# Kernel optimization log

Measured on AMD Instinct MI355X. Metric: run time of the kernel, lower is better.

## Reference

```python
import jax, jax.numpy as jnp
import numpy as np

EPS_LAM = 1e-6
GN_GROUPS = 4
GN_EPS = 1e-5


def _conv(x, k):
    # x: (N, Cin, H, W), k: (Cout, Cin, 3, 3), SAME padding, stride 1
    return jax.lax.conv_general_dilated(x, k, (1, 1), 'SAME',
                                        dimension_numbers=('NCHW', 'OIHW', 'NCHW'))


def _clifford_conv(x, wa, wb, ba, bb):
    # Cl(0,1) (complex-style) Clifford conv: channels split into two blade components.
    C = x.shape[1]
    h = C // 2
    a, b = x[:, :h], x[:, h:]
    oa = _conv(a, wa) - _conv(b, wb) + ba[None, :, None, None]
    ob = _conv(a, wb) + _conv(b, wa) + bb[None, :, None, None]
    return jnp.concatenate([oa, ob], axis=1)


def _helmholtz(x):
    # Project the vector field (vx = first half of channels, vy = second half)
    # onto its divergence-free component in Fourier space.
    N, C, H, W = x.shape
    h = C // 2
    vx, vy = x[:, :h], x[:, h:]
    kx = jnp.fft.rfftfreq(W)[None, :]   # (1, FW)
    ky = jnp.fft.fftfreq(H)[:, None]    # (H, 1)
    k2 = kx * kx + ky * ky              # (H, FW)
    vxh = jnp.fft.rfft2(vx, norm='ortho')
    vyh = jnp.fft.rfft2(vy, norm='ortho')
    num = kx * vxh + ky * vyh
    p = jnp.where(k2 == 0, 0.0, num / jnp.where(k2 == 0, 1.0, k2))
    vxp = jnp.fft.irfft2(vxh - kx * p, s=(H, W), norm='ortho')
    vyp = jnp.fft.irfft2(vyh - ky * p, s=(H, W), norm='ortho')
    return jnp.concatenate([vxp, vyp], axis=1)


def _group_norm(x, w, b):
    N, C, H, W = x.shape
    xg = x.reshape(N, GN_GROUPS, -1)
    mu = xg.mean(-1, keepdims=True)
    var = xg.var(-1, keepdims=True)
    xn = ((xg - mu) * jax.lax.rsqrt(var + GN_EPS)).reshape(N, C, H, W)
    return xn * w[None, :, None, None] + b[None, :, None, None]


def setup_inputs() -> dict:
    key = jax.random.key(0)
    ks = jax.random.split(key, 6)
    B, T, C, H, W = 2, 16, 128, 64, 64
    hC = C // 2
    sc = 0.05
    return {
        'x_seq': jax.random.normal(ks[0], (B, T, C, H, W), jnp.float32),
        'dt_seq': jax.random.uniform(ks[1], (B, T), jnp.float32, 0.05, 1.0),
        'gen_w': jax.random.normal(ks[2], (C, 2 * C), jnp.float32) * (1.0 / np.sqrt(C)),
        'gen_b': jnp.zeros((2 * C,), jnp.float32),
        'cw_a': jax.random.normal(ks[3], (hC, hC, 3, 3), jnp.float32) * sc,
        'cw_b': jax.random.normal(ks[4], (hC, hC, 3, 3), jnp.float32) * sc,
        'cb_a': jnp.zeros((hC,), jnp.float32),
        'cb_b': jnp.zeros((hC,), jnp.float32),
        'gn_w': jnp.ones((C,), jnp.float32),
        'gn_b': jnp.zeros((C,), jnp.float32),
    }


def reference(x_seq, dt_seq, gen_w, gen_b, cw_a, cw_b, cb_a, cb_b, gn_w, gn_b):
    B, T, C, H, W = x_seq.shape
    dt = dt_seq[:, :, None, None, None]                   # (B,T,1,1,1)
    x_fft = jnp.fft.rfft2(x_seq, norm='ortho')            # (B,T,C,H,FW) complex64
    stats = x_seq.mean(axis=(-1, -2))                     # (B,T,C)
    params = stats @ gen_w + gen_b                        # (B,T,2C)
    nu, omega = jnp.split(params, 2, axis=-1)
    lam = (-jnp.abs(nu) + 1j * omega)[:, :, :, None, None]  # (B,T,C,1,1)
    A_scan = jnp.exp(lam * dt)
    small = jnp.abs(lam) < EPS_LAM
    safe = jnp.where(small, jnp.complex64(EPS_LAM), lam)
    X_term = jnp.where(small, dt.astype(jnp.complex64), (jnp.exp(safe * dt) - 1.0) / safe)
    X = (x_fft * X_term).astype(jnp.complex64)            # (B,T,C,H,FW)
    A = jnp.broadcast_to(A_scan.astype(jnp.complex64), X.shape)

    def comb(l, r):
        al, xl = l
        ar, xr = r
        return (al * ar, ar * xl + xr)

    _, h_fft = jax.lax.associative_scan(comb, (A, X), axis=1)  # h_t = A_t h_{t-1} + X_t
    h = jnp.fft.irfft2(h_fft, s=(H, W), norm='ortho')
    hf = h.reshape(B * T, C, H, W)
    u = hf + _clifford_conv(hf, cw_a, cw_b, cb_a, cb_b)
    u = _helmholtz(u)
    out = _group_norm(u, gn_w, gn_b)
    return out.reshape(B, T, C, H, W)
```

## Files before the change

kernel.cpp:

```cpp
#include <hip/hip_runtime.h>
#include <math.h>

#define PI_F 3.14159265358979323846f
#define ST 66

typedef __attribute__((ext_vector_type(8))) short short8;
typedef __attribute__((ext_vector_type(4))) float f32x4;
typedef __attribute__((ext_vector_type(4))) unsigned short u16x4;
typedef __attribute__((ext_vector_type(8))) unsigned short u16x8;

static __device__ __forceinline__ int sw(int row, int intra) {
    return row * ST + (intra ^ (row & 7));
}

static __device__ __forceinline__ unsigned short f2bf(float x) {
    unsigned u = __float_as_uint(x);
    unsigned r = (u + 0x7FFF + ((u >> 16) & 1)) >> 16;
    return (unsigned short)r;
}
static __device__ __forceinline__ float bf2f(unsigned short u) {
    return __uint_as_float(((unsigned)u) << 16);
}
static __device__ __forceinline__ float2 unpk(unsigned v) {
    return make_float2(bf2f((unsigned short)(v & 0xffff)), bf2f((unsigned short)(v >> 16)));
}

static __device__ __forceinline__ float2 cadd(float2 a, float2 b) { return make_float2(a.x + b.x, a.y + b.y); }
static __device__ __forceinline__ float2 csub(float2 a, float2 b) { return make_float2(a.x - b.x, a.y - b.y); }
static __device__ __forceinline__ float2 cmul(float2 a, float2 b) { return make_float2(a.x * b.x - a.y * b.y, a.x * b.y + a.y * b.x); }
static __device__ __forceinline__ float2 cmulc(float2 a, float2 b) { return make_float2(a.x * b.x + a.y * b.y, a.y * b.x - a.x * b.y); }

template <int S>
static __device__ __forceinline__ void dft8(float2* z) {
    const float RT = 0.70710678118654752440f;
    float2 ee0 = cadd(z[0], z[4]), ee1 = csub(z[0], z[4]);
    float2 eo0 = cadd(z[2], z[6]), eo1 = csub(z[2], z[6]);
    float2 oe0 = cadd(z[1], z[5]), oe1 = csub(z[1], z[5]);
    float2 oo0 = cadd(z[3], z[7]), oo1 = csub(z[3], z[7]);
    float2 ieo1 = make_float2(-S * eo1.y, S * eo1.x);
    float2 ioo1 = make_float2(-S * oo1.y, S * oo1.x);
    float2 E0 = cadd(ee0, eo0), E2 = csub(ee0, eo0);
    float2 E1 = cadd(ee1, ieo1), E3 = csub(ee1, ieo1);
    float2 O0 = cadd(oe0, oo0), O2 = csub(oe0, oo0);
    float2 O1 = cadd(oe1, ioo1), O3 = csub(oe1, ioo1);
    float2 w1O1 = make_float2(RT * (O1.x - S * O1.y), RT * (S * O1.x + O1.y));
    float2 w3O3 = make_float2(RT * (-O3.x - S * O3.y), RT * (S * O3.x - O3.y));
    float2 iO2  = make_float2(-S * O2.y, S * O2.x);
    z[0] = cadd(E0, O0);   z[4] = csub(E0, O0);
    z[1] = cadd(E1, w1O1); z[5] = csub(E1, w1O1);
    z[2] = cadd(E2, iO2);  z[6] = csub(E2, iO2);
    z[3] = cadd(E3, w3O3); z[7] = csub(E3, w3O3);
}

template <int S>
static __device__ __forceinline__ void fftRowsA(float2* G, const float2* twl, int tid) {
#pragma unroll
    for (int sl = 0; sl < 2; ++sl) {
        int s = tid + sl * 256;
        int row = s >> 3, b = s & 7;
        float2 z[8];
#pragma unroll
        for (int a = 0; a < 8; ++a) z[a] = G[sw(row, 8 * a + b)];
        dft8<S>(z);
#pragma unroll
        for (int c = 0; c < 8; ++c) {
            float2 t = twl[(b * c) & 63];
            G[sw(row, 8 * c + b)] = (S < 0) ? cmul(z[c], t) : cmulc(z[c], t);
        }
    }
}
template <int S>
static __device__ __forceinline__ void fftRowsB(float2* G, int tid) {
    int r0 = tid >> 3, c = tid & 7, r1 = r0 + 32;
    float2 z0[8], z1[8];
#pragma unroll
    for (int b = 0; b < 8; ++b) z0[b] = G[sw(r0, 8 * c + b)];
#pragma unroll
    for (int b = 0; b < 8; ++b) z1[b] = G[sw(r1, 8 * c + b)];
    dft8<S>(z0); dft8<S>(z1);
    __syncthreads();
#pragma unroll
    for (int d = 0; d < 8; ++d) G[sw(r0, c + 8 * d)] = z0[d];
#pragma unroll
    for (int d = 0; d < 8; ++d) G[sw(r1, c + 8 * d)] = z1[d];
}
template <int S>
static __device__ __forceinline__ void fftColsA(float2* G, const float2* twl, int tid) {
#pragma unroll
    for (int sl = 0; sl < 2; ++sl) {
        int s = tid + sl * 256;
        int col = s & 63, b = s >> 6;
        float2 z[8];
#pragma unroll
        for (int a = 0; a < 8; ++a) z[a] = G[sw(8 * a + b, col)];
        dft8<S>(z);
#pragma unroll
        for (int c = 0; c < 8; ++c) {
            float2 t = twl[(b * c) & 63];
            G[sw(8 * c + b, col)] = (S < 0) ? cmul(z[c], t) : cmulc(z[c], t);
        }
    }
}
template <int S>
static __device__ __forceinline__ void fftColsB(float2* G, int tid) {
    int col = tid & 63, c0 = tid >> 6, c1 = c0 + 4;
    float2 z0[8], z1[8];
#pragma unroll
    for (int b = 0; b < 8; ++b) z0[b] = G[sw(8 * c0 + b, col)];
#pragma unroll
    for (int b = 0; b < 8; ++b) z1[b] = G[sw(8 * c1 + b, col)];
    dft8<S>(z0); dft8<S>(z1);
    __syncthreads();
#pragma unroll
    for (int d = 0; d < 8; ++d) G[sw(c0 + 8 * d, col)] = z0[d];
#pragma unroll
    for (int d = 0; d < 8; ++d) G[sw(c1 + 8 * d, col)] = z1[d];
}

__global__ __launch_bounds__(256) void k_params(const float* __restrict__ stats,
                                                const float* __restrict__ gw,
                                                const float* __restrict__ gb,
                                                const float* __restrict__ dts,
                                                float2* __restrict__ A,
                                                float2* __restrict__ Xt) {
    int idx = blockIdx.x * 256 + threadIdx.x;
    int c = idx & 127;
    int bt = idx >> 7;
    const float* st = stats + bt * 128;
    float nu = gb[c], om = gb[c + 128];
    for (int k = 0; k < 128; ++k) {
        float s = st[k];
        nu += s * gw[k * 256 + c];
        om += s * gw[k * 256 + c + 128];
    }
    float dt = dts[bt];
    float lre = -fabsf(nu);
    float lim = om;
    float mag = sqrtf(lre * lre + lim * lim);
    float er = expf(lre * dt);
    float sn, cs;
    sincosf(lim * dt, &sn, &cs);
    float2 Av = make_float2(er * cs, er * sn);
    float2 X;
    if (mag < 1e-6f) {
        X = make_float2(dt, 0.f);
    } else {
        float ar = Av.x - 1.f, ai = Av.y;
        float inv = 1.f / (mag * mag);
        X = make_float2((ar * lre + ai * lim) * inv, (ai * lre - ar * lim) * inv);
    }
    A[idx] = Av;
    Xt[idx] = X;
}

__global__ __launch_bounds__(256) void k_rfft2s(const float* __restrict__ xin,
                                                unsigned* __restrict__ Sb,
                                                float* __restrict__ stats) {
    int p = blockIdx.x, tid = threadIdx.x;
    __shared__ float2 G[64 * ST], twl[64];
    __shared__ float red[8];
    if (tid < 64) {
        float sn, cs;
        sincosf(-(2.0f * PI_F / 64.0f) * (float)tid, &sn, &cs);
        twl[tid] = make_float2(cs, sn);
    }
    const float* x0 = xin + (size_t)(2 * p) * 4096;
    const float* x1 = x0 + 4096;
    float s0 = 0.f, s1 = 0.f;
    for (int i4 = tid; i4 < 1024; i4 += 256) {
        float4 a = ((const float4*)x0)[i4];
        float4 b = ((const float4*)x1)[i4];
        s0 += a.x + a.y + a.z + a.w;
        s1 += b.x + b.y + b.z + b.w;
        int r = i4 >> 4, w = (i4 & 15) << 2;
        G[sw(r, w + 0)] = make_float2(a.x, b.x);
        G[sw(r, w + 1)] = make_float2(a.y, b.y);
        G[sw(r, w + 2)] = make_float2(a.z, b.z);
        G[sw(r, w + 3)] = make_float2(a.w, b.w);
    }
    for (int off = 32; off > 0; off >>= 1) {
        s0 += __shfl_xor(s0, off, 64);
        s1 += __shfl_xor(s1, off, 64);
    }
    if ((tid & 63) == 0) { red[(tid >> 6) * 2] = s0; red[(tid >> 6) * 2 + 1] = s1; }
    __syncthreads();
    if (tid < 2) {
        float t = red[tid] + red[tid + 2] + red[tid + 4] + red[tid + 6];
        stats[2 * p + tid] = t * (1.0f / 4096.0f);
    }
    fftRowsA<-1>(G, twl, tid); __syncthreads();
    fftRowsB<-1>(G, tid);      __syncthreads();
    fftColsA<-1>(G, twl, tid); __syncthreads();
    fftColsB<-1>(G, tid);      __syncthreads();

    unsigned* o0 = Sb + (size_t)(2 * p) * 2112;
    unsigned* o1 = o0 + 2112;
    for (int i = tid; i < 2112; i += 256) {
        int my = i / 33, mx = i - my * 33;
        float2 Zk = G[sw(my, mx)];
        float2 Zm = G[sw((64 - my) & 63, (64 - mx) & 63)];
        float a0 = (Zk.x + Zm.x) * (0.5f / 64.0f);
        float a1 = (Zk.y - Zm.y) * (0.5f / 64.0f);
        float b0 = (Zk.y + Zm.y) * (0.5f / 64.0f);
        float b1 = (Zm.x - Zk.x) * (0.5f / 64.0f);
        o0[i] = (unsigned)f2bf(a0) | ((unsigned)f2bf(a1) << 16);
        o1[i] = (unsigned)f2bf(b0) | ((unsigned)f2bf(b1) << 16);
    }
}

typedef __attribute__((ext_vector_type(2))) unsigned uint2v;
__global__ __launch_bounds__(256) void k_scan(unsigned* __restrict__ Sb,
                                              const float2* __restrict__ A,
                                              const float2* __restrict__ Xt) {
    int tid = blockIdx.x * 256 + threadIdx.x;
    int s = tid % 1056;
    int c = (tid / 1056) & 127;
    int b = tid / (1056 * 128);
    float2 h0 = make_float2(0.f, 0.f), h1 = make_float2(0.f, 0.f);
    for (int t = 0; t < 16; ++t) {
        int bt = b * 16 + t;
        float2 a = A[bt * 128 + c];
        float2 xt = Xt[bt * 128 + c];
        size_t off = ((size_t)(bt * 128 + c)) * 2112 + 2 * s;
        uint2v v = *(uint2v*)(Sb + off);
        float2 x0 = cmul(unpk(v[0]), xt);
        float2 x1 = cmul(unpk(v[1]), xt);
        h0 = make_float2(a.x * h0.x - a.y * h0.y + x0.x, a.x * h0.y + a.y * h0.x + x0.y);
        h1 = make_float2(a.x * h1.x - a.y * h1.y + x1.x, a.x * h1.y + a.y * h1.x + x1.y);
        uint2v o;
        o[0] = (unsigned)f2bf(h0.x) | ((unsigned)f2bf(h0.y) << 16);
        o[1] = (unsigned)f2bf(h1.x) | ((unsigned)f2bf(h1.y) << 16);
        *(uint2v*)(Sb + off) = o;
    }
}

__global__ __launch_bounds__(256) void k_irfft2b(const unsigned* __restrict__ Sb,
                                                 unsigned short* __restrict__ hb) {
    int p = blockIdx.x, tid = threadIdx.x;
    __shared__ float2 G[64 * ST], twl[64];
    if (tid < 64) {
        float sn, cs;
        sincosf(-(2.0f * PI_F / 64.0f) * (float)tid, &sn, &cs);
        twl[tid] = make_float2(cs, sn);
    }
    const unsigned* i0 = Sb + (size_t)(2 * p) * 2112;
    const unsigned* i1 = i0 + 2112;
    for (int i = tid; i < 1984; i += 256) {
        int mx = 1 + i % 31, my = i / 31;
        int idx = my * 33 + mx;
        float2 a = unpk(i0[idx]);
        float2 b = unpk(i1[idx]);
        G[sw(my, mx)] = make_float2(a.x - b.y, a.y + b.x);
        G[sw((64 - my) & 63, 64 - mx)] = make_float2(a.x + b.y, b.x - a.y);
    }
    if (tid < 64) {
        int mx = (tid >= 32) ? 32 : 0;
        int r = tid & 31;
        if (r == 0) {
#pragma unroll
            for (int q = 0; q < 2; ++q) {
                int my = q * 32;
                float2 a = unpk(i0[my * 33 + mx]);
                float2 b = unpk(i1[my * 33 + mx]);
                G[sw(my, mx)] = make_float2(a.x, b.x);
            }
        } else {
            int my = r, my2 = 64 - r;
            float2 A0 = unpk(i0[my * 33 + mx]),  B0 = unpk(i0[my2 * 33 + mx]);
            float2 A1 = unpk(i1[my * 33 + mx]),  B1 = unpk(i1[my2 * 33 + mx]);
            float2 V0 = make_float2((A0.x + B0.x) * 0.5f, (A0.y - B0.y) * 0.5f);
            float2 V1 = make_float2((A1.x + B1.x) * 0.5f, (A1.y - B1.y) * 0.5f);
            G[sw(my, mx)]  = make_float2(V0.x - V1.y, V0.y + V1.x);
            G[sw(my2, mx)] = make_float2(V0.x + V1.y, V1.x - V0.y);
        }
    }
    __syncthreads();
    fftColsA<1>(G, twl, tid); __syncthreads();
    fftColsB<1>(G, tid);      __syncthreads();
    fftRowsA<1>(G, twl, tid); __syncthreads();
    fftRowsB<1>(G, tid);      __syncthreads();

    unsigned short* h0 = hb + (size_t)(2 * p) * 4096;
    unsigned short* h1 = h0 + 4096;
    for (int i4 = tid; i4 < 1024; i4 += 256) {
        int r = i4 >> 4, w = (i4 & 15) << 2;
        u16x4 oa, ob;
#pragma unroll
        for (int e = 0; e < 4; ++e) {
            float2 v = G[sw(r, w + e)];
            oa[e] = f2bf(v.x * (1.0f / 64.0f));
            ob[e] = f2bf(v.y * (1.0f / 64.0f));
        }
        ((u16x4*)h0)[i4] = oa;
        ((u16x4*)h1)[i4] = ob;
    }
}

__global__ __launch_bounds__(256) void k_wprep(const float* __restrict__ cwa,
                                               const float* __restrict__ cwb,
                                               unsigned short* __restrict__ Wb) {
    int idx = blockIdx.x * 256 + threadIdx.x;
    int kl = idx & 31;
    int m = (idx >> 5) & 127;
    int tcb = idx >> 12;
    int cb = tcb & 3, t = tcb >> 2;
    int ci = cb * 32 + kl;
    int mm = m & 63, cc = ci & 63;
    float w;
    if (m < 64) w = (ci < 64) ? cwa[(mm * 64 + cc) * 9 + t] : -cwb[(mm * 64 + cc) * 9 + t];
    else        w = (ci < 64) ? cwb[(mm * 64 + cc) * 9 + t] :  cwa[(mm * 64 + cc) * 9 + t];
    if (m == ci && t == 4) w += 1.0f;
    Wb[idx] = f2bf(w);
}

__global__ __launch_bounds__(256, 2) void k_conv_mfma(const unsigned short* __restrict__ hb,
                                                      const unsigned short* __restrict__ Wb,
                                                      const float* __restrict__ cba,
                                                      const float* __restrict__ cbb,
                                                      unsigned short* __restrict__ uout) {
    __shared__ __align__(16) char smem[65536];
    int f = blockIdx.y;
    int r0 = blockIdx.x * 2;
    int tid = threadIdx.x;
    const unsigned short* base = hb + (size_t)f * 524288;

    int wid = tid >> 6, lane = tid & 63;
    int lhi = lane >> 4, llo = lane & 15;
    int row_off = wid & 1;
    int mbase = (wid >> 1) * 64;

    auto ldA = [&](int t, int cb, short8* a) {
        const unsigned short* wp = Wb + ((size_t)((t * 4 + cb) * 128 + mbase + llo)) * 32 + lhi * 8;
#pragma unroll
        for (int mf = 0; mf < 4; ++mf) a[mf] = *(const short8*)(wp + mf * 16 * 32);
    };
    auto ldB = [&](int t, int cb, short8* b) {
        int dy = t / 3 - 1, dx = t % 3 - 1;
        int prow = row_off + 1 + dy;
        int slot = cb * 4 + lhi;
#pragma unroll
        for (int nf = 0; nf < 4; ++nf) {
            int c = nf * 16 + llo;
            int cdx = c + dx;
            bool valid = ((unsigned)cdx < 64u);
            int cr = valid ? cdx : c;
            int byteoff = ((prow * 64 + cr) << 8) + ((slot ^ (cr & 15)) << 4);
            short8 bb = *(const short8*)(smem + byteoff);
            b[nf] = valid ? bb : (short8)0;
        }
    };

    short8 aC[4], bC[4], aN[4], bN[4];
    ldA(0, 0, aC);

    for (int j = tid; j < 4096; j += 256) {
        int row = j >> 10;
        int cig = (j >> 6) & 15;
        int col = j & 63;
        int gr = r0 - 1 + row;
        short8 v = (short8)0;
        if ((unsigned)gr < 64u) {
            const unsigned short* p = base + (size_t)(cig * 8) * 4096 + gr * 64 + col;
#pragma unroll
            for (int e = 0; e < 8; ++e) v[e] = (short)p[(size_t)e * 4096];
        }
        int byteoff = ((row * 64 + col) << 8) + ((cig ^ (col & 15)) << 4);
        *(short8*)(smem + byteoff) = v;
    }
    __syncthreads();

    f32x4 acc[4][4];
#pragma unroll
    for (int mf = 0; mf < 4; ++mf)
#pragma unroll
        for (int nf = 0; nf < 4; ++nf) acc[mf][nf] = (f32x4)0.f;

    ldB(0, 0, bC);
#pragma unroll
    for (int it = 0; it < 36; ++it) {
        if (it < 35) {
            int tn = (it + 1) >> 2, cbn = (it + 1) & 3;
            ldA(tn, cbn, aN);
            ldB(tn, cbn, bN);
        }
        __builtin_amdgcn_s_setprio(1);
#pragma unroll
        for (int mf = 0; mf < 4; ++mf)
#pragma unroll
            for (int nf = 0; nf < 4; ++nf)
                acc[mf][nf] = __builtin_amdgcn_mfma_f32_16x16x32_bf16(aC[mf], bC[nf], acc[mf][nf], 0, 0, 0);
        __builtin_amdgcn_s_setprio(0);
#pragma unroll
        for (int k = 0; k < 4; ++k) { aC[k] = aN[k]; bC[k] = bN[k]; }
    }

    int grow = r0 + row_off;
#pragma unroll
    for (int mf = 0; mf < 4; ++mf) {
#pragma unroll
        for (int r = 0; r < 4; ++r) {
            int co = mbase + mf * 16 + lhi * 4 + r;
            float bias = (co < 64) ? cba[co] : cbb[co - 64];
            unsigned short* op = uout + ((size_t)f * 128 + co) * 4096 + (size_t)grow * 64;
#pragma unroll
            for (int nf = 0; nf < 4; ++nf)
                op[nf * 16 + llo] = f2bf(acc[mf][nf][r] + bias);
        }
    }
}

__global__ __launch_bounds__(256) void k_helm(const unsigned short* __restrict__ uin,
                                              unsigned short* __restrict__ uo,
                                              float* __restrict__ partials) {
    int bid = blockIdx.x;
    int f = bid >> 6, c = bid & 63;
    int tid = threadIdx.x;
    __shared__ float2 G[64 * ST], twl[64];
    __shared__ float red[16];
    if (tid < 64) {
        float sn, cs;
        sincosf(-(2.0f * PI_F / 64.0f) * (float)tid, &sn, &cs);
        twl[tid] = make_float2(cs, sn);
    }
    const unsigned short* u0 = uin + ((size_t)f * 128 + c) * 4096;
    const unsigned short* u1 = u0 + (size_t)64 * 4096;
    for (int i4 = tid; i4 < 1024; i4 += 256) {
        u16x4 a = ((const u16x4*)u0)[i4];
        u16x4 b = ((const u16x4*)u1)[i4];
        int r = i4 >> 4, w = (i4 & 15) << 2;
#pragma unroll
        for (int e = 0; e < 4; ++e)
            G[sw(r, w + e)] = make_float2(bf2f(a[e]), bf2f(b[e]));
    }
    __syncthreads();
    fftRowsA<-1>(G, twl, tid); __syncthreads();
    fftRowsB<-1>(G, tid);      __syncthreads();
    fftColsA<-1>(G, twl, tid); __syncthreads();
    fftColsB<-1>(G, tid);      __syncthreads();

    for (int i = tid; i < 1984; i += 256) {
        int mx = 1 + i % 31, my = i / 31;
        float2 Zk = G[sw(my, mx)];
        float2 Zm = G[sw((64 - my) & 63, 64 - mx)];
        float2 Vx = make_float2((Zk.x + Zm.x) * 0.5f, (Zk.y - Zm.y) * 0.5f);
        float2 Vy = make_float2((Zk.y + Zm.y) * 0.5f, (Zm.x - Zk.x) * 0.5f);
        float fx = (float)mx * (1.0f / 64.0f);
        float fy = (float)(my < 32 ? my : my - 64) * (1.0f / 64.0f);
        float inv = 1.0f / (fx * fx + fy * fy);
        float Pr = (fx * Vx.x + fy * Vy.x) * inv;
        float Pi = (fx * Vx.y + fy * Vy.y) * inv;
        Vx.x -= fx * Pr; Vx.y -= fx * Pi;
        Vy.x -= fy * Pr; Vy.y -= fy * Pi;
        G[sw(my, mx)] = make_float2(Vx.x - Vy.y, Vx.y + Vy.x);
        G[sw((64 - my) & 63, 64 - mx)] = make_float2(Vx.x + Vy.y, Vy.x - Vx.y);
    }
    if (tid < 64) {
        int mx = (tid >= 32) ? 32 : 0;
        int r = tid & 31;
        float fx = (float)mx * (1.0f / 64.0f);
        if (r == 0) {
#pragma unroll
            for (int q = 0; q < 2; ++q) {
                int my = q * 32;
                float fy = (my == 0) ? 0.f : -0.5f;
                float k2 = fx * fx + fy * fy;
                float2 Z = G[sw(my, mx)];
                float vx = Z.x, vy = Z.y;
                if (k2 > 0.f) {
                    float P = (fx * vx + fy * vy) / k2;
                    vx -= fx * P; vy -= fy * P;
                }
                G[sw(my, mx)] = make_float2(vx, vy);
            }
        } else {
            int my = r, my2 = 64 - r;
            float fy = (float)my * (1.0f / 64.0f);
            float inv = 1.0f / (fx * fx + fy * fy);
            float2 Zk = G[sw(my, mx)];
            float2 Zm = G[sw(my2, mx)];
            float2 Vx = make_float2((Zk.x + Zm.x) * 0.5f, (Zk.y - Zm.y) * 0.5f);
            float2 Vy = make_float2((Zk.y + Zm.y) * 0.5f, (Zm.x - Zk.x) * 0.5f);
            float Pr = (fx * Vx.x + fy * Vy.x) * inv;
            float Pi = (fx * Vx.y + fy * Vy.y) * inv;
            float2 Xk = make_float2(Vx.x - fx * Pr, Vx.y - fx * Pi);
            float2 Yk = make_float2(Vy.x - fy * Pr, Vy.y - fy * Pi);
            float P2r = (fx * Vx.x - fy * Vy.x) * inv;
            float P2i = (-fx * Vx.y + fy * Vy.y) * inv;
            float2 Xk2 = make_float2(Vx.x - fx * P2r, -Vx.y - fx * P2i);
            float2 Yk2 = make_float2(Vy.x + fy * P2r, -Vy.y + fy * P2i);
            float2 Xh = make_float2((Xk.x + Xk2.x) * 0.5f, (Xk.y - Xk2.y) * 0.5f);
            float2 Yh = make_float2((Yk.x + Yk2.x) * 0.5f, (Yk.y - Yk2.y) * 0.5f);
            G[sw(my, mx)]  = make_float2(Xh.x - Yh.y, Xh.y + Yh.x);
            G[sw(my2, mx)] = make_float2(Xh.x + Yh.y, Yh.x - Xh.y);
        }
    }
    __syncthreads();
    fftColsA<1>(G, twl, tid); __syncthreads();
    fftColsB<1>(G, tid);      __syncthreads();
    fftRowsA<1>(G, twl, tid); __syncthreads();
    fftRowsB<1>(G, tid);      __syncthreads();

    unsigned short* o0 = uo + ((size_t)f * 128 + c) * 4096;
    unsigned short* o1 = o0 + (size_t)64 * 4096;
    float s0 = 0.f, q0 = 0.f, s1 = 0.f, q1 = 0.f;
    for (int i4 = tid; i4 < 1024; i4 += 256) {
        int r = i4 >> 4, w = (i4 & 15) << 2;
        u16x4 oa, ob;
#pragma unroll
        for (int e = 0; e < 4; ++e) {
            float2 v = G[sw(r, w + e)];
            float a = v.x * (1.0f / 4096.0f);
            float b = v.y * (1.0f / 4096.0f);
            s0 += a; q0 += a * a; s1 += b; q1 += b * b;
            oa[e] = f2bf(a); ob[e] = f2bf(b);
        }
        ((u16x4*)o0)[i4] = oa;
        ((u16x4*)o1)[i4] = ob;
    }
    for (int off = 32; off > 0; off >>= 1) {
        s0 += __shfl_xor(s0, off, 64); q0 += __shfl_xor(q0, off, 64);
        s1 += __shfl_xor(s1, off, 64); q1 += __shfl_xor(q1, off, 64);
    }
    if ((tid & 63) == 0) {
        int w6 = tid >> 6;
        red[w6 * 4 + 0] = s0; red[w6 * 4 + 1] = q0;
        red[w6 * 4 + 2] = s1; red[w6 * 4 + 3] = q1;
    }
    __syncthreads();
    if (tid == 0) {
        float S0 = 0.f, Q0 = 0.f, S1 = 0.f, Q1 = 0.f;
#pragma unroll
        for (int w6 = 0; w6 < 4; ++w6) {
            S0 += red[w6 * 4 + 0]; Q0 += red[w6 * 4 + 1];
            S1 += red[w6 * 4 + 2]; Q1 += red[w6 * 4 + 3];
        }
        float* pp = partials + ((size_t)f * 64 + c) * 4;
        pp[0] = S0; pp[1] = Q0; pp[2] = S1; pp[3] = Q1;
    }
}

__global__ __launch_bounds__(128) void k_gnfin(const float* __restrict__ partials,
                                               float2* __restrict__ gs) {
    int i = threadIdx.x;
    int f = i >> 2, g = i & 3;
    const float4* p4 = (const float4*)partials;
    float s = 0.f, q = 0.f;
    if (g < 2) {
        for (int cc = 0; cc < 32; ++cc) {
            float4 p = p4[f * 64 + g * 32 + cc];
            s += p.x; q += p.y;
        }
    } else {
        for (int cc = 0; cc < 32; ++cc) {
            float4 p = p4[f * 64 + (g - 2) * 32 + cc];
            s += p.z; q += p.w;
        }
    }
    float mu = s * (1.0f / 131072.0f);
    float var = q * (1.0f / 131072.0f) - mu * mu;
    gs[i] = make_float2(mu, rsqrtf(var + 1e-5f));
}

__global__ __launch_bounds__(256) void k_gnapply(const unsigned short* __restrict__ u,
                                                 const float2* __restrict__ gs,
                                                 const float* __restrict__ gnw,
                                                 const float* __restrict__ gnb,
                                                 float* __restrict__ out) {
    size_t i8 = (size_t)blockIdx.x * 256 + threadIdx.x;
    u16x8 v = ((const u16x8*)u)[i8];
    int cl = (int)(i8 >> 9);
    int c = cl & 127;
    int fg = cl >> 5;
    float2 ms = gs[fg];
    float sc = ms.y * gnw[c];
    float sh = gnb[c] - ms.x * sc;
    float4 r0, r1;
    r0.x = bf2f(v[0]) * sc + sh; r0.y = bf2f(v[1]) * sc + sh;
    r0.z = bf2f(v[2]) * sc + sh; r0.w = bf2f(v[3]) * sc + sh;
    r1.x = bf2f(v[4]) * sc + sh; r1.y = bf2f(v[5]) * sc + sh;
    r1.z = bf2f(v[6]) * sc + sh; r1.w = bf2f(v[7]) * sc + sh;
    ((float4*)out)[i8 * 2]     = r0;
    ((float4*)out)[i8 * 2 + 1] = r1;
}

extern "C" void kernel_launch(void* const* d_in, const int* in_sizes, int n_in,
                              void* d_out, int out_size, void* d_ws, size_t ws_size,
                              hipStream_t stream) {
    (void)in_sizes; (void)n_in; (void)out_size; (void)ws_size;
    const float* x   = (const float*)d_in[0];
    const float* dts = (const float*)d_in[1];
    const float* gw  = (const float*)d_in[2];
    const float* gb  = (const float*)d_in[3];
    const float* cwa = (const float*)d_in[4];
    const float* cwb = (const float*)d_in[5];
    const float* cba = (const float*)d_in[6];
    const float* cbb = (const float*)d_in[7];
    const float* gnw = (const float*)d_in[8];
    const float* gnb = (const float*)d_in[9];
    float* out = (float*)d_out;
    char* ws = (char*)d_ws;

    unsigned*       Sb  = (unsigned*)ws;
    unsigned short* Hb  = (unsigned short*)(ws + 34603008);
    unsigned short* Ub  = (unsigned short*)(ws + 68157440);
    unsigned short* H1b = (unsigned short*)(ws + 101711872);
    float*  stats    = (float*)(ws + 135266304);
    float2* A        = (float2*)(ws + 135282688);
    float2* Xt       = (float2*)(ws + 135315456);
    float2* gs       = (float2*)(ws + 135348224);
    float*  partials = (float*)(ws + 135349248);
    unsigned short* Wb = (unsigned short*)ws;

    k_rfft2s<<<2048, 256, 0, stream>>>(x, Sb, stats);
    k_params<<<16, 256, 0, stream>>>(stats, gw, gb, dts, A, Xt);
    k_scan<<<1056, 256, 0, stream>>>(Sb, A, Xt);
    k_irfft2b<<<2048, 256, 0, stream>>>(Sb, Hb);
    k_wprep<<<576, 256, 0, stream>>>(cwa, cwb, Wb);
    k_conv_mfma<<<dim3(32, 32), 256, 0, stream>>>(Hb, Wb, cba, cbb, Ub);
    k_helm<<<2048, 256, 0, stream>>>(Ub, H1b, partials);
    k_gnfin<<<1, 128, 0, stream>>>(partials, gs);
    k_gnapply<<<8192, 256, 0, stream>>>(H1b, gs, gnw, gnb, out);
}
```

Baseline: 213.0 us.

## Make 2D FFT passes wave-local to replace block barriers with wave syncs

Reassigns FFT work so each wavefront owns 16 complete rows (or columns) and does both radix-8 stages on them. The intermediate block-wide barriers inside each 1D pass become wave-level LDS waitcnt fences, and the load/store loops are remapped so each wave touches only its own rows. This removes several __syncthreads per FFT in the rfft, irfft and Helmholtz kernels, and adds per-wave twiddle copies plus a rotated column read order to reduce bank conflicts. The risk is that correctness now depends on the wave-size and LDS-ordering assumptions behind wave_sync.

```diff
diff --git a/kernel.cpp b/kernel.cpp
--- a/kernel.cpp
+++ b/kernel.cpp
@@ -8,9 +8,15 @@
 typedef __attribute__((ext_vector_type(4))) float f32x4;
 typedef __attribute__((ext_vector_type(4))) unsigned short u16x4;
 typedef __attribute__((ext_vector_type(8))) unsigned short u16x8;
+typedef __attribute__((ext_vector_type(2))) unsigned uint2v;
 
 static __device__ __forceinline__ int sw(int row, int intra) {
     return row * ST + (intra ^ (row & 7));
+}
+
+static __device__ __forceinline__ void wave_sync() {
+    asm volatile("s_waitcnt lgkmcnt(0)" ::: "memory");
+    __builtin_amdgcn_sched_barrier(0);
 }
 
 static __device__ __forceinline__ unsigned short f2bf(float x) {
@@ -53,11 +59,12 @@
 }
 
 template <int S>
-static __device__ __forceinline__ void fftRowsA(float2* G, const float2* twl, int tid) {
+static __device__ __forceinline__ void waveRows(float2* G, const float2* twl, int w, int lane) {
+    int lr = lane >> 3, b = lane & 7;
+    int r0 = 16 * w + lr;
 #pragma unroll
     for (int sl = 0; sl < 2; ++sl) {
-        int s = tid + sl * 256;
-        int row = s >> 3, b = s & 7;
+        int row = r0 + 8 * sl;
         float2 z[8];
 #pragma unroll
         for (int a = 0; a < 8; ++a) z[a] = G[sw(row, 8 * a + b)];
@@ -68,28 +75,29 @@
             G[sw(row, 8 * c + b)] = (S < 0) ? cmul(z[c], t) : cmulc(z[c], t);
         }
     }
+    wave_sync();
+    {
+        int c = b;
+        float2 z0[8], z1[8];
+#pragma unroll
+        for (int q = 0; q < 8; ++q) z0[q] = G[sw(r0, c * 8 + q)];
+#pragma unroll
+        for (int q = 0; q < 8; ++q) z1[q] = G[sw(r0 + 8, c * 8 + q)];
+        dft8<S>(z0); dft8<S>(z1);
+        wave_sync();
+#pragma unroll
+        for (int d = 0; d < 8; ++d) G[sw(r0, c + 8 * d)] = z0[d];
+#pragma unroll
+        for (int d = 0; d < 8; ++d) G[sw(r0 + 8, c + 8 * d)] = z1[d];
+    }
 }
 template <int S>
-static __device__ __forceinline__ void fftRowsB(float2* G, int tid) {
-    int r0 = tid >> 3, c = tid & 7, r1 = r0 + 32;
-    float2 z0[8], z1[8];
-#pragma unroll
-    for (int b = 0; b < 8; ++b) z0[b] = G[sw(r0, 8 * c + b)];
-#pragma unroll
-    for (int b = 0; b < 8; ++b) z1[b] = G[sw(r1, 8 * c + b)];
-    dft8<S>(z0); dft8<S>(z1);
-    __syncthreads();
-#pragma unroll
-    for (int d = 0; d < 8; ++d) G[sw(r0, c + 8 * d)] = z0[d];
-#pragma unroll
-    for (int d = 0; d < 8; ++d) G[sw(r1, c + 8 * d)] = z1[d];
-}
-template <int S>
-static __device__ __forceinline__ void fftColsA(float2* G, const float2* twl, int tid) {
+static __device__ __forceinline__ void waveCols(float2* G, const float2* twl, int w, int lane) {
+    int cl = lane >> 3, b = lane & 7;
+    int c0 = 16 * w + cl;
 #pragma unroll
     for (int sl = 0; sl < 2; ++sl) {
-        int s = tid + sl * 256;
-        int col = s & 63, b = s >> 6;
+        int col = c0 + 8 * sl;
         float2 z[8];
 #pragma unroll
         for (int a = 0; a < 8; ++a) z[a] = G[sw(8 * a + b, col)];
@@ -100,21 +108,27 @@
             G[sw(8 * c + b, col)] = (S < 0) ? cmul(z[c], t) : cmulc(z[c], t);
         }
     }
-}
-template <int S>
-static __device__ __forceinline__ void fftColsB(float2* G, int tid) {
-    int col = tid & 63, c0 = tid >> 6, c1 = c0 + 4;
-    float2 z0[8], z1[8];
-#pragma unroll
-    for (int b = 0; b < 8; ++b) z0[b] = G[sw(8 * c0 + b, col)];
-#pragma unroll
-    for (int b = 0; b < 8; ++b) z1[b] = G[sw(8 * c1 + b, col)];
-    dft8<S>(z0); dft8<S>(z1);
-    __syncthreads();
-#pragma unroll
-    for (int d = 0; d < 8; ++d) G[sw(c0 + 8 * d, col)] = z0[d];
-#pragma unroll
-    for (int d = 0; d < 8; ++d) G[sw(c1 + 8 * d, col)] = z1[d];
+    wave_sync();
+    {
+        int cidx = b;
+        float2 z0[8], z1[8];
+#pragma unroll
+        for (int q = 0; q < 8; ++q) {
+            int b2 = (q + cidx) & 7;
+            z0[b2] = G[sw(8 * cidx + b2, c0)];
+        }
+#pragma unroll
+        for (int q = 0; q < 8; ++q) {
+            int b2 = (q + cidx) & 7;
+            z1[b2] = G[sw(8 * cidx + b2, c0 + 8)];
+        }
+        dft8<S>(z0); dft8<S>(z1);
+        wave_sync();
+#pragma unroll
+        for (int d = 0; d < 8; ++d) G[sw(cidx + 8 * d, c0)] = z0[d];
+#pragma unroll
+        for (int d = 0; d < 8; ++d) G[sw(cidx + 8 * d, c0 + 8)] = z1[d];
+    }
 }
 
 __global__ __launch_bounds__(256) void k_params(const float* __restrict__ stats,
@@ -157,6 +171,7 @@
                                                 unsigned* __restrict__ Sb,
                                                 float* __restrict__ stats) {
     int p = blockIdx.x, tid = threadIdx.x;
+    int w = tid >> 6, lane = tid & 63;
     __shared__ float2 G[64 * ST], twl[64];
     __shared__ float red[8];
     if (tid < 64) {
@@ -172,26 +187,26 @@
         float4 b = ((const float4*)x1)[i4];
         s0 += a.x + a.y + a.z + a.w;
         s1 += b.x + b.y + b.z + b.w;
-        int r = i4 >> 4, w = (i4 & 15) << 2;
-        G[sw(r, w + 0)] = make_float2(a.x, b.x);
-        G[sw(r, w + 1)] = make_float2(a.y, b.y);
-        G[sw(r, w + 2)] = make_float2(a.z, b.z);
-        G[sw(r, w + 3)] = make_float2(a.w, b.w);
+        int r = i4 >> 4, wv = (i4 & 15) << 2;
+        G[sw(r, wv + 0)] = make_float2(a.x, b.x);
+        G[sw(r, wv + 1)] = make_float2(a.y, b.y);
+        G[sw(r, wv + 2)] = make_float2(a.z, b.z);
+        G[sw(r, wv + 3)] = make_float2(a.w, b.w);
     }
     for (int off = 32; off > 0; off >>= 1) {
         s0 += __shfl_xor(s0, off, 64);
         s1 += __shfl_xor(s1, off, 64);
     }
-    if ((tid & 63) == 0) { red[(tid >> 6) * 2] = s0; red[(tid >> 6) * 2 + 1] = s1; }
+    if (lane == 0) { red[w * 2] = s0; red[w * 2 + 1] = s1; }
     __syncthreads();
     if (tid < 2) {
         float t = red[tid] + red[tid + 2] + red[tid + 4] + red[tid + 6];
         stats[2 * p + tid] = t * (1.0f / 4096.0f);
     }
-    fftRowsA<-1>(G, twl, tid); __syncthreads();
-    fftRowsB<-1>(G, tid);      __syncthreads();
-    fftColsA<-1>(G, twl, tid); __syncthreads();
-    fftColsB<-1>(G, tid);      __syncthreads();
+    waveRows<-1>(G, twl, w, lane);
+    __syncthreads();
+    waveCols<-1>(G, twl, w, lane);
+    __syncthreads();
 
     unsigned* o0 = Sb + (size_t)(2 * p) * 2112;
     unsigned* o1 = o0 + 2112;
@@ -208,7 +223,6 @@
     }
 }
 
-typedef __attribute__((ext_vector_type(2))) unsigned uint2v;
 __global__ __launch_bounds__(256) void k_scan(unsigned* __restrict__ Sb,
                                               const float2* __restrict__ A,
                                               const float2* __restrict__ Xt) {
@@ -237,6 +251,7 @@
 __global__ __launch_bounds__(256) void k_irfft2b(const unsigned* __restrict__ Sb,
                                                  unsigned short* __restrict__ hb) {
     int p = blockIdx.x, tid = threadIdx.x;
+    int w = tid >> 6, lane = tid & 63;
     __shared__ float2 G[64 * ST], twl[64];
     if (tid < 64) {
         float sn, cs;
@@ -275,24 +290,24 @@
         }
     }
     __syncthreads();
-    fftColsA<1>(G, twl, tid); __syncthreads();
-    fftColsB<1>(G, tid);      __syncthreads();
-    fftRowsA<1>(G, twl, tid); __syncthreads();
-    fftRowsB<1>(G, tid);      __syncthreads();
+    waveCols<1>(G, twl, w, lane);
+    __syncthreads();
+    waveRows<1>(G, twl, w, lane);
+    wave_sync();
 
     unsigned short* h0 = hb + (size_t)(2 * p) * 4096;
     unsigned short* h1 = h0 + 4096;
-    for (int i4 = tid; i4 < 1024; i4 += 256) {
-        int r = i4 >> 4, w = (i4 & 15) << 2;
+    for (int j = lane; j < 256; j += 64) {
+        int row = 16 * w + (j >> 4), ch = j & 15;
         u16x4 oa, ob;
 #pragma unroll
         for (int e = 0; e < 4; ++e) {
-            float2 v = G[sw(r, w + e)];
+            float2 v = G[sw(row, ch * 4 + e)];
             oa[e] = f2bf(v.x * (1.0f / 64.0f));
             ob[e] = f2bf(v.y * (1.0f / 64.0f));
         }
-        ((u16x4*)h0)[i4] = oa;
-        ((u16x4*)h1)[i4] = ob;
+        ((u16x4*)h0)[row * 16 + ch] = oa;
+        ((u16x4*)h1)[row * 16 + ch] = ob;
     }
 }
 
@@ -415,28 +430,31 @@
     int bid = blockIdx.x;
     int f = bid >> 6, c = bid & 63;
     int tid = threadIdx.x;
-    __shared__ float2 G[64 * ST], twl[64];
+    int w = tid >> 6, lane = tid & 63;
+    __shared__ float2 G[64 * ST], twl4[256];
     __shared__ float red[16];
-    if (tid < 64) {
+    {
         float sn, cs;
-        sincosf(-(2.0f * PI_F / 64.0f) * (float)tid, &sn, &cs);
-        twl[tid] = make_float2(cs, sn);
-    }
+        sincosf(-(2.0f * PI_F / 64.0f) * (float)lane, &sn, &cs);
+        twl4[w * 64 + lane] = make_float2(cs, sn);
+    }
+    const float2* twl = twl4 + w * 64;
+
     const unsigned short* u0 = uin + ((size_t)f * 128 + c) * 4096;
     const unsigned short* u1 = u0 + (size_t)64 * 4096;
-    for (int i4 = tid; i4 < 1024; i4 += 256) {
-        u16x4 a = ((const u16x4*)u0)[i4];
-        u16x4 b = ((const u16x4*)u1)[i4];
-        int r = i4 >> 4, w = (i4 & 15) << 2;
+    for (int j = lane; j < 256; j += 64) {
+        int row = 16 * w + (j >> 4), ch = j & 15;
+        u16x4 a = ((const u16x4*)u0)[row * 16 + ch];
+        u16x4 b = ((const u16x4*)u1)[row * 16 + ch];
 #pragma unroll
         for (int e = 0; e < 4; ++e)
-            G[sw(r, w + e)] = make_float2(bf2f(a[e]), bf2f(b[e]));
-    }
-    __syncthreads();
-    fftRowsA<-1>(G, twl, tid); __syncthreads();
-    fftRowsB<-1>(G, tid);      __syncthreads();
-    fftColsA<-1>(G, twl, tid); __syncthreads();
-    fftColsB<-1>(G, tid);      __syncthreads();
+            G[sw(row, ch * 4 + e)] = make_float2(bf2f(a[e]), bf2f(b[e]));
+    }
+    wave_sync();
+    waveRows<-1>(G, twl, w, lane);
+    __syncthreads();
+    waveCols<-1>(G, twl, w, lane);
+    __syncthreads();
 
     for (int i = tid; i < 1984; i += 256) {
         int mx = 1 + i % 31, my = i / 31;
@@ -495,36 +513,35 @@
         }
     }
     __syncthreads();
-    fftColsA<1>(G, twl, tid); __syncthreads();
-    fftColsB<1>(G, tid);      __syncthreads();
-    fftRowsA<1>(G, twl, tid); __syncthreads();
-    fftRowsB<1>(G, tid);      __syncthreads();
+    waveCols<1>(G, twl, w, lane);
+    __syncthreads();
+    waveRows<1>(G, twl, w, lane);
+    wave_sync();
 
     unsigned short* o0 = uo + ((size_t)f * 128 + c) * 4096;
     unsigned short* o1 = o0 + (size_t)64 * 4096;
     float s0 = 0.f, q0 = 0.f, s1 = 0.f, q1 = 0.f;
-    for (int i4 = tid; i4 < 1024; i4 += 256) {
-        int r = i4 >> 4, w = (i4 & 15) << 2;
+    for (int j = lane; j < 256; j += 64) {
+        int row = 16 * w + (j >> 4), ch = j & 15;
         u16x4 oa, ob;
 #pragma unroll
         for (int e = 0; e < 4; ++e) {
-            float2 v = G[sw(r, w + e)];
+            float2 v = G[sw(row, ch * 4 + e)];
             float a = v.x * (1.0f / 4096.0f);
             float b = v.y * (1.0f / 4096.0f);
             s0 += a; q0 += a * a; s1 += b; q1 += b * b;
             oa[e] = f2bf(a); ob[e] = f2bf(b);
         }
-        ((u16x4*)o0)[i4] = oa;
-        ((u16x4*)o1)[i4] = ob;
+        ((u16x4*)o0)[row * 16 + ch] = oa;
+        ((u16x4*)o1)[row * 16 + ch] = ob;
     }
     for (int off = 32; off > 0; off >>= 1) {
         s0 += __shfl_xor(s0, off, 64); q0 += __shfl_xor(q0, off, 64);
         s1 += __shfl_xor(s1, off, 64); q1 += __shfl_xor(q1, off, 64);
     }
-    if ((tid & 63) == 0) {
-        int w6 = tid >> 6;
-        red[w6 * 4 + 0] = s0; red[w6 * 4 + 1] = q0;
-        red[w6 * 4 + 2] = s1; red[w6 * 4 + 3] = q1;
+    if (lane == 0) {
+        red[w * 4 + 0] = s0; red[w * 4 + 1] = q0;
+        red[w * 4 + 2] = s1; red[w * 4 + 3] = q1;
     }
     __syncthreads();
     if (tid == 0) {
```

After: 363.9 us. 70.9% more time.
